# Kernel tuning notes

Hardware: AMD Instinct MI355X
Metric: run time of the kernel (lower is better)

The kernel has to match this reference:

```python
import jax, jax.numpy as jnp
import numpy as np

N_NODES = 100000
N_EDGES = 1600000
F_IN, F_HID, F_OUT = 128, 128, 16
NEG_SLOPE = 0.2


def _glorot(key, shape):
    fan = sum(shape)
    return jax.random.uniform(key, shape, jnp.float32, -1.0, 1.0) * jnp.sqrt(6.0 / fan)


def setup_inputs() -> dict:
    key = jax.random.key(0)
    ks = jax.random.split(key, 16)
    x = jax.random.normal(ks[0], (N_NODES, F_IN), jnp.float32)
    edge_index = jax.random.randint(ks[1], (2, N_EDGES), 0, N_NODES, jnp.int64)
    d1, d2, d3 = F_HID, F_HID // 2, F_OUT
    return {
        'x': x,
        'edge_index': edge_index,
        'W1': _glorot(ks[2], (F_IN, d1)), 'a_src1': _glorot(ks[3], (d1,)), 'a_dst1': _glorot(ks[4], (d1,)), 'b1': jnp.zeros((d1,), jnp.float32),
        'W2': _glorot(ks[5], (d1, d2)), 'a_src2': _glorot(ks[6], (d2,)), 'a_dst2': _glorot(ks[7], (d2,)), 'b2': jnp.zeros((d2,), jnp.float32),
        'W3': _glorot(ks[8], (d2, d3)), 'a_src3': _glorot(ks[9], (d3,)), 'a_dst3': _glorot(ks[10], (d3,)), 'b3': jnp.zeros((d3,), jnp.float32),
    }


def gat_conv(x, src, dst, W, a_s, a_d, b):
    # x: [N, Fin] -> h: [N, Fout]; src/dst: [E] (self-loops included)
    h = x @ W
    e = jax.nn.leaky_relu(h @ a_s, NEG_SLOPE * 0 + NEG_SLOPE)  # placeholder avoided below
    # attention logits per edge: leaky_relu(alpha_src[src] + alpha_dst[dst])
    al_s = h @ a_s  # [N]
    al_d = h @ a_d  # [N]
    logits = jax.nn.leaky_relu(al_s[src] + al_d[dst], NEG_SLOPE)  # [E]
    # numerically stable softmax over incoming edges of each dst node
    m = jax.ops.segment_max(logits, dst, num_segments=N_NODES)
    m = jnp.where(jnp.isfinite(m), m, 0.0)
    ex = jnp.exp(logits - m[dst])
    denom = jax.ops.segment_sum(ex, dst, num_segments=N_NODES)
    alpha = ex / denom[dst]  # self-loops guarantee denom > 0
    out = jax.ops.segment_sum(alpha[:, None] * h[src], dst, num_segments=N_NODES)
    return out + b


def reference(x, edge_index, W1, a_src1, a_dst1, b1, W2, a_src2, a_dst2, b2, W3, a_src3, a_dst3, b3):
    loops = jnp.arange(N_NODES, dtype=edge_index.dtype)
    src = jnp.concatenate([edge_index[0], loops])
    dst = jnp.concatenate([edge_index[1], loops])
    h = gat_conv(x, src, dst, W1, a_src1, a_dst1, b1)
    h = jax.nn.relu(h)  # dropout p=0.5 is identity in eval mode
    h = gat_conv(h, src, dst, W2, a_src2, a_dst2, b2)
    h = jax.nn.relu(h)
    out = gat_conv(h, src, dst, W3, a_src3, a_dst3, b3)
    return out
```

## Files before the change

### kernel.cpp

```cpp
#include <hip/hip_runtime.h>
#include <hip/hip_bf16.h>

typedef __hip_bfloat16 bf16;
typedef __attribute__((ext_vector_type(8))) __bf16 bf16x8;
typedef __attribute__((ext_vector_type(4))) float f32x4;

static constexpr int N = 100000;
static constexpr int E = 1600000;
static constexpr int ETOT = E + N;
static constexpr float SLOPE = 0.2f;

__device__ __constant__ int c_poff[12] = {0, 16384, 16512, 16640,
                                          16768, 24960, 25024, 25088,
                                          25152, 26176, 26192, 26208};
static constexpr int PTOT = 26224;
static constexpr int H_POFF[12] = {0, 16384, 16512, 16640, 16768, 24960,
                                   25024, 25088, 25152, 26176, 26192, 26208};

struct Src12 { const void* p[12]; };

__device__ __forceinline__ float bfLo(unsigned u) { return __uint_as_float(u << 16); }
__device__ __forceinline__ float bfHi(unsigned u) { return __uint_as_float(u & 0xFFFF0000u); }

__device__ __forceinline__ void fma8(const uint4 r, float e, float* acc) {
  acc[0] = fmaf(e, bfLo(r.x), acc[0]);
  acc[1] = fmaf(e, bfHi(r.x), acc[1]);
  acc[2] = fmaf(e, bfLo(r.y), acc[2]);
  acc[3] = fmaf(e, bfHi(r.y), acc[3]);
  acc[4] = fmaf(e, bfLo(r.z), acc[4]);
  acc[5] = fmaf(e, bfHi(r.z), acc[5]);
  acc[6] = fmaf(e, bfLo(r.w), acc[6]);
  acc[7] = fmaf(e, bfHi(r.w), acc[7]);
}

__device__ __forceinline__ float edge_ex(float l) {
  l = (l > 0.f) ? l : SLOPE * l;
  return __expf(l);
}

__device__ __forceinline__ void loadEdge(const int* __restrict__ ei32,
                                         const long long* __restrict__ ei64,
                                         int use64, int t, int& s, int& d) {
  if (t >= E) { s = d = t - E; return; }
  if (use64) { s = (int)ei64[t]; d = (int)ei64[E + t]; }
  else       { s = ei32[t];      d = ei32[E + t]; }
}

__device__ __forceinline__ unsigned pk2(float a, float b) {
  bf16 x = __float2bfloat16(a), y = __float2bfloat16(b);
  unsigned short ux = *(unsigned short*)&x, uy = *(unsigned short*)&y;
  return ((unsigned)uy << 16) | ux;
}

static constexpr int CHUNK = 8192;
static constexpr int NCHK  = (ETOT + CHUNK - 1) / CHUNK;
static constexpr int NB1   = (N + 511) / 512;
static constexpr int M1    = NB1 * NCHK;
static constexpr int SBLK  = (M1 + 255) / 256;

__global__ __launch_bounds__(256) void detect_kernel(
    const unsigned long long* __restrict__ ei64,
    const unsigned short* __restrict__ w1u16, int* __restrict__ flags) {
  const int t = threadIdx.x;
  __shared__ unsigned long long bl[4];
  __shared__ unsigned long long sb64;
  const int w = t >> 6;
  bool p64 = (t < 64) && (ei64[t] >= (unsigned long long)N);
  unsigned long long b64 = __ballot(p64);
  if (t == 0) sb64 = b64;
  bool pf = (((w1u16[t] >> 7) & 0xFFu) >= 126u);
  unsigned long long bf_ = __ballot(pf);
  if ((t & 63) == 0) bl[w] = bf_;
  __syncthreads();
  if (t == 0) {
    flags[0] = (sb64 == 0ull) ? 1 : 0;
    flags[1] = ((bl[0] | bl[1] | bl[2] | bl[3]) != 0ull) ? 1 : 0;
  }
}

static constexpr int PB_PAR = (PTOT + 255) / 256;
static constexpr int PB_W1  = 128 * 128 / 256;
static constexpr int PB_W2  = 128 * 64 / 256;
static constexpr int PB_W3  = 64 * 16 / 256;
static constexpr int PB_TOT = NCHK + PB_PAR + PB_W1 + PB_W2 + PB_W3;

__device__ __forceinline__ void conv_w(const void* W, int kd, int dout, int f32,
                                       bf16* __restrict__ wt, int idx) {
  int n = idx / kd, k = idx - n * kd;
  float v = f32 ? ((const float*)W)[k * dout + n]
                : __bfloat162float(((const bf16*)W)[k * dout + n]);
  wt[idx] = __float2bfloat16(v);
}

__global__ __launch_bounds__(256) void prep_kernel(
    const int* __restrict__ ei32, const long long* __restrict__ ei64,
    const int* __restrict__ flags, int* __restrict__ c1,
    Src12 s, float* __restrict__ prm,
    bf16* __restrict__ w1t, bf16* __restrict__ w2t, bf16* __restrict__ w3t) {
  const int b = blockIdx.x, tid = threadIdx.x;
  const int f64 = flags[0], f32 = flags[1];
  if (b < NCHK) {
    __shared__ int h1[NB1];
    if (tid < NB1) h1[tid] = 0;
    __syncthreads();
    const int t0 = b * CHUNK;
#pragma unroll 4
    for (int i = tid; i < CHUNK; i += 256) {
      int t = t0 + i;
      if (t < ETOT) {
        int d = (t >= E) ? (t - E) : (f64 ? (int)ei64[E + t] : ei32[E + t]);
        atomicAdd(&h1[d >> 9], 1);
      }
    }
    __syncthreads();
    if (tid < NB1) c1[tid * NCHK + b] = h1[tid];
  } else if (b < NCHK + PB_PAR) {
    int t = (b - NCHK) * 256 + tid;
    if (t < PTOT) {
      int k = 0;
#pragma unroll
      for (int i = 1; i < 12; ++i)
        if (t >= c_poff[i]) k = i;
      int j = t - c_poff[k];
      prm[t] = f32 ? ((const float*)s.p[k])[j]
                   : __bfloat162float(((const bf16*)s.p[k])[j]);
    }
  } else if (b < NCHK + PB_PAR + PB_W1) {
    conv_w(s.p[0], 128, 128, f32, w1t, (b - NCHK - PB_PAR) * 256 + tid);
  } else if (b < NCHK + PB_PAR + PB_W1 + PB_W2) {
    conv_w(s.p[4], 128, 64, f32, w2t, (b - NCHK - PB_PAR - PB_W1) * 256 + tid);
  } else {
    conv_w(s.p[8], 64, 16, f32, w3t, (b - NCHK - PB_PAR - PB_W1 - PB_W2) * 256 + tid);
  }
}

__global__ __launch_bounds__(256) void scanA_kernel(const int* __restrict__ c1,
                                                    int* __restrict__ bsum) {
  __shared__ int red[256];
  const int t = threadIdx.x;
  const int i = blockIdx.x * 256 + t;
  red[t] = (i < M1) ? c1[i] : 0;
  __syncthreads();
#pragma unroll
  for (int off = 128; off > 0; off >>= 1) {
    if (t < off) red[t] += red[t + off];
    __syncthreads();
  }
  if (t == 0) bsum[blockIdx.x] = red[0];
}

__global__ __launch_bounds__(256) void scanB_kernel(const int* __restrict__ bsum,
                                                    int* __restrict__ boff) {
  __shared__ int s[256];
  const int t = threadIdx.x;
  const int v = (t < SBLK) ? bsum[t] : 0;
  s[t] = v;
  __syncthreads();
  for (int off = 1; off < 256; off <<= 1) {
    int u = (t >= off) ? s[t - off] : 0;
    __syncthreads();
    s[t] += u;
    __syncthreads();
  }
  if (t < SBLK) boff[t] = s[t] - v;
}

__global__ __launch_bounds__(256) void scanC_kernel(const int* __restrict__ c1,
                                                    const int* __restrict__ boff,
                                                    int* __restrict__ off1) {
  __shared__ int s[256];
  const int t = threadIdx.x;
  const int i = blockIdx.x * 256 + t;
  const int v = (i < M1) ? c1[i] : 0;
  s[t] = v;
  __syncthreads();
#pragma unroll
  for (int off = 1; off < 256; off <<= 1) {
    int u = (t >= off) ? s[t - off] : 0;
    __syncthreads();
    s[t] += u;
    __syncthreads();
  }
  if (i < M1) off1[i] = boff[blockIdx.x] + s[t] - v;
}

__device__ __forceinline__ void phaseC_body(int c, const int* __restrict__ ei32,
                                            const long long* __restrict__ ei64,
                                            int f64, const int* __restrict__ off1,
                                            int2* __restrict__ tmp) {
  __shared__ int cur[NB1];
  const int tid = threadIdx.x;
  if (tid < NB1) cur[tid] = off1[tid * NCHK + c];
  __syncthreads();
  const int t0 = c * CHUNK;
#pragma unroll 4
  for (int i = tid; i < CHUNK; i += 256) {
    int t = t0 + i;
    if (t < ETOT) {
      int s, d;
      loadEdge(ei32, ei64, f64, t, s, d);
      int pos = atomicAdd(&cur[d >> 9], 1);
      tmp[pos] = make_int2(d, s);
    }
  }
}

__global__ __launch_bounds__(256) void phaseD_kernel(const int* __restrict__ off1,
                                                     const int2* __restrict__ tmp,
                                                     int* __restrict__ rowptr,
                                                     int* __restrict__ ssrt) {
  __shared__ int h2[512], e2[512], cur[512];
  __shared__ int ps[256];
  const int b = blockIdx.x, t = threadIdx.x;
  const int base = off1[b * NCHK];
  const int end = (b + 1 < NB1) ? off1[(b + 1) * NCHK] : ETOT;
  const int len = end - base;
  h2[2 * t] = 0; h2[2 * t + 1] = 0;
  __syncthreads();
  for (int i = t; i < len; i += 256)
    atomicAdd(&h2[tmp[base + i].x & 511], 1);
  __syncthreads();
  const int s1 = h2[2 * t], s2 = h2[2 * t + 1];
  ps[t] = s1 + s2;
  __syncthreads();
  for (int off = 1; off < 256; off <<= 1) {
    int u = (t >= off) ? ps[t - off] : 0;
    __syncthreads();
    ps[t] += u;
    __syncthreads();
  }
  const int ep = ps[t] - (s1 + s2);
  e2[2 * t] = ep;
  e2[2 * t + 1] = ep + s1;
  cur[2 * t] = ep;
  cur[2 * t + 1] = ep + s1;
  __syncthreads();
#pragma unroll
  for (int k = 0; k < 2; ++k) {
    int f = 2 * t + k;
    int node = (b << 9) + f;
    if (node < N) rowptr[node] = base + e2[f];
  }
  if (b == 0 && t == 0) rowptr[N] = ETOT;
  for (int i = t; i < len; i += 256) {
    int2 e = tmp[base + i];
    int pos = base + atomicAdd(&cur[e.x & 511], 1);
    ssrt[pos] = e.y;
  }
}

template <int KD, int DOUT, bool XD>
__device__ __forceinline__ void gemm_body(int bb, const void* __restrict__ inv,
                                          const int* __restrict__ flags,
                                          const unsigned short* __restrict__ wt,
                                          bf16* __restrict__ h,
                                          const float* __restrict__ a_s,
                                          const float* __restrict__ a_d,
                                          float* __restrict__ als,
                                          float* __restrict__ ald) {
  constexpr int SA = KD + 8;
  constexpr int NT = DOUT / 16;
  constexpr int KS = KD / 32;
  __shared__ unsigned short sA[64 * SA];
  __shared__ unsigned short sB[DOUT * SA];
  const int tid = threadIdx.x;
  const int m0 = bb * 64;
  for (int idx = tid; idx < DOUT * KD / 8; idx += 256) {
    int n = idx / (KD / 8), k8 = idx - n * (KD / 8);
    *(uint4*)(sB + n * SA + k8 * 8) = *(const uint4*)(wt + n * KD + k8 * 8);
  }
  const bool f32 = XD ? (flags[1] != 0) : false;
  for (int idx = tid; idx < 64 * KD / 8; idx += 256) {
    int r = idx / (KD / 8), k8 = idx - r * (KD / 8);
    int m = m0 + r;
    uint4 v = make_uint4(0, 0, 0, 0);
    if (m < N) {
      if (XD && f32) {
        const float4 v0 = *((const float4*)inv + ((size_t)m * KD + k8 * 8) / 4);
        const float4 v1 = *((const float4*)inv + ((size_t)m * KD + k8 * 8) / 4 + 1);
        v = make_uint4(pk2(v0.x, v0.y), pk2(v0.z, v0.w),
                       pk2(v1.x, v1.y), pk2(v1.z, v1.w));
      } else {
        v = *((const uint4*)inv + ((size_t)m * KD + k8 * 8) / 8);
      }
    }
    *(uint4*)(sA + r * SA + k8 * 8) = v;
  }
  __syncthreads();
  const int lane = tid & 63;
  const int wv = tid >> 6;
  const int lr = lane & 15;
  const int q = lane >> 4;
  f32x4 acc[NT];
#pragma unroll
  for (int t = 0; t < NT; ++t)
#pragma unroll
    for (int r = 0; r < 4; ++r) acc[t][r] = 0.f;
  const int arow = wv * 16 + lr;
#pragma unroll
  for (int ks = 0; ks < KS; ++ks) {
    const int k0 = ks * 32 + q * 8;
    const bf16x8 a = *(const bf16x8*)(sA + arow * SA + k0);
#pragma unroll
    for (int t = 0; t < NT; ++t) {
      const bf16x8 b = *(const bf16x8*)(sB + (t * 16 + lr) * SA + k0);
      acc[t] = __builtin_amdgcn_mfma_f32_16x16x32_bf16(a, b, acc[t], 0, 0, 0);
    }
  }
  float ps[4] = {0.f, 0.f, 0.f, 0.f}, pd[4] = {0.f, 0.f, 0.f, 0.f};
#pragma unroll
  for (int t = 0; t < NT; ++t) {
    const float av = a_s[t * 16 + lr];
    const float dv = a_d[t * 16 + lr];
#pragma unroll
    for (int r = 0; r < 4; ++r) {
      ps[r] = fmaf(acc[t][r], av, ps[r]);
      pd[r] = fmaf(acc[t][r], dv, pd[r]);
    }
  }
#pragma unroll
  for (int m = 1; m < 16; m <<= 1)
#pragma unroll
    for (int r = 0; r < 4; ++r) {
      ps[r] += __shfl_xor(ps[r], m, 64);
      pd[r] += __shfl_xor(pd[r], m, 64);
    }
  const int mb = m0 + wv * 16 + q * 4;
  if (lr == 0) {
#pragma unroll
    for (int r = 0; r < 4; ++r) {
      int m = mb + r;
      if (m < N) { als[m] = ps[r]; ald[m] = pd[r]; }
    }
  }
#pragma unroll
  for (int t = 0; t < NT; ++t)
#pragma unroll
    for (int r = 0; r < 4; ++r) {
      int m = mb + r;
      if (m < N) h[(size_t)m * DOUT + t * 16 + lr] = __float2bfloat16(acc[t][r]);
    }
}

static constexpr int GB1 = (N + 63) / 64;

__global__ __launch_bounds__(256) void gemm1_phaseC(
    const void* __restrict__ x, const int* __restrict__ flags,
    const unsigned short* __restrict__ wt, bf16* __restrict__ h,
    const float* __restrict__ a_s, const float* __restrict__ a_d,
    float* __restrict__ als, float* __restrict__ ald,
    const int* __restrict__ ei32, const long long* __restrict__ ei64,
    const int* __restrict__ off1, int2* __restrict__ tmp) {
  if (blockIdx.x < GB1) {
    gemm_body<128, 128, true>(blockIdx.x, x, flags, wt, h, a_s, a_d, als, ald);
  } else {
    int c = blockIdx.x - GB1;
    if (c < NCHK) phaseC_body(c, ei32, ei64, flags[0], off1, tmp);
  }
}

template <int KD, int DOUT>
__global__ __launch_bounds__(256, 8) void agg_gemm(
    const int* __restrict__ rowptr, const int* __restrict__ ssrt,
    const float* __restrict__ als_in, const float* __restrict__ ald_in,
    const unsigned short* __restrict__ hb, const float* __restrict__ bias_in,
    const unsigned short* __restrict__ wt, bf16* __restrict__ hout,
    const float* __restrict__ a_s, const float* __restrict__ a_d,
    float* __restrict__ als_out, float* __restrict__ ald_out) {
  constexpr int SA = KD + 8;
  constexpr int NT = DOUT / 16;
  constexpr int KS = KD / 32;
  constexpr int TPN = KD / 8;
  constexpr int NPB = 256 / TPN;
  constexpr int NBAT = 64 / NPB;
  __shared__ unsigned short sA[64 * SA];
  const int tid = threadIdx.x;
  const int m0 = blockIdx.x * 64;
  const int sub = tid % TPN;
  const int rb = tid / TPN;
  const int col0 = sub * 8;
#pragma unroll
  for (int bat = 0; bat < NBAT; ++bat) {
    const int r = bat * NPB + rb;
    const int d = m0 + r;
    uint4 w = make_uint4(0, 0, 0, 0);
    if (d < N) {
      const int p0 = rowptr[d], p1 = rowptr[d + 1];
      const float ad = ald_in[d];
      float acc[8];
#pragma unroll
      for (int c = 0; c < 8; ++c) acc[c] = 0.f;
      float sum = 0.f;
      int p = p0;
      for (; p + 4 <= p1; p += 4) {
        const int s0 = ssrt[p + 0];
        const int s1 = ssrt[p + 1];
        const int s2 = ssrt[p + 2];
        const int s3 = ssrt[p + 3];
        const uint4 r0 = *reinterpret_cast<const uint4*>(hb + (size_t)s0 * KD + col0);
        const uint4 r1 = *reinterpret_cast<const uint4*>(hb + (size_t)s1 * KD + col0);
        const uint4 r2 = *reinterpret_cast<const uint4*>(hb + (size_t)s2 * KD + col0);
        const uint4 r3 = *reinterpret_cast<const uint4*>(hb + (size_t)s3 * KD + col0);
        const float x0 = edge_ex(als_in[s0] + ad);
        const float x1 = edge_ex(als_in[s1] + ad);
        const float x2 = edge_ex(als_in[s2] + ad);
        const float x3 = edge_ex(als_in[s3] + ad);
        sum += (x0 + x1) + (x2 + x3);
        fma8(r0, x0, acc);
        fma8(r1, x1, acc);
        fma8(r2, x2, acc);
        fma8(r3, x3, acc);
      }
      for (; p < p1; ++p) {
        const int s = ssrt[p];
        const uint4 rr = *reinterpret_cast<const uint4*>(hb + (size_t)s * KD + col0);
        const float x = edge_ex(als_in[s] + ad);
        sum += x;
        fma8(rr, x, acc);
      }
      const float inv = 1.f / sum;
      float v[8];
#pragma unroll
      for (int c = 0; c < 8; ++c) {
        float t = acc[c] * inv + bias_in[col0 + c];
        v[c] = (t > 0.f) ? t : 0.f;
      }
      w = make_uint4(pk2(v[0], v[1]), pk2(v[2], v[3]),
                     pk2(v[4], v[5]), pk2(v[6], v[7]));
    }
    *(uint4*)(sA + r * SA + col0) = w;
  }
  __syncthreads();
  const int lane = tid & 63;
  const int wv = tid >> 6;
  const int lr = lane & 15;
  const int q = lane >> 4;
  f32x4 acc[NT];
#pragma unroll
  for (int t = 0; t < NT; ++t)
#pragma unroll
    for (int r = 0; r < 4; ++r) acc[t][r] = 0.f;
  const int arow = wv * 16 + lr;
#pragma unroll
  for (int ks = 0; ks < KS; ++ks) {
    const int k0 = ks * 32 + q * 8;
    const bf16x8 a = *(const bf16x8*)(sA + arow * SA + k0);
#pragma unroll
    for (int t = 0; t < NT; ++t) {
      const bf16x8 b = *(const bf16x8*)(wt + (t * 16 + lr) * KD + k0);
      acc[t] = __builtin_amdgcn_mfma_f32_16x16x32_bf16(a, b, acc[t], 0, 0, 0);
    }
  }
  float ps[4] = {0.f, 0.f, 0.f, 0.f}, pd[4] = {0.f, 0.f, 0.f, 0.f};
#pragma unroll
  for (int t = 0; t < NT; ++t) {
    const float av = a_s[t * 16 + lr];
    const float dv = a_d[t * 16 + lr];
#pragma unroll
    for (int r = 0; r < 4; ++r) {
      ps[r] = fmaf(acc[t][r], av, ps[r]);
      pd[r] = fmaf(acc[t][r], dv, pd[r]);
    }
  }
#pragma unroll
  for (int m = 1; m < 16; m <<= 1)
#pragma unroll
    for (int r = 0; r < 4; ++r) {
      ps[r] += __shfl_xor(ps[r], m, 64);
      pd[r] += __shfl_xor(pd[r], m, 64);
    }
  const int mb = m0 + wv * 16 + q * 4;
  if (lr == 0) {
#pragma unroll
    for (int r = 0; r < 4; ++r) {
      int m = mb + r;
      if (m < N) { als_out[m] = ps[r]; ald_out[m] = pd[r]; }
    }
  }
#pragma unroll
  for (int t = 0; t < NT; ++t)
#pragma unroll
    for (int r = 0; r < 4; ++r) {
      int m = mb + r;
      if (m < N) hout[(size_t)m * DOUT + t * 16 + lr] = __float2bfloat16(acc[t][r]);
    }
}

template <int DOUT, bool RELU, bool FINAL>
__global__ __launch_bounds__(256) void aggregate_csr(const int* __restrict__ rowptr,
                                                     const int* __restrict__ ssrt,
                                                     const float* __restrict__ als,
                                                     const float* __restrict__ ald,
                                                     const unsigned short* __restrict__ hb,
                                                     const float* __restrict__ bias,
                                                     bf16* __restrict__ outb,
                                                     void* __restrict__ outv,
                                                     const int* __restrict__ flags) {
  constexpr int TPN = DOUT / 8;
  constexpr int NPB = 256 / TPN;
  const int sub = threadIdx.x % TPN;
  const int d = blockIdx.x * NPB + threadIdx.x / TPN;
  if (d >= N) return;
  const int p0 = rowptr[d], p1 = rowptr[d + 1];
  const float ad = ald[d];
  const int col0 = sub * 8;
  float acc[8];
#pragma unroll
  for (int c = 0; c < 8; ++c) acc[c] = 0.f;
  float sum = 0.f;
  int p = p0;
  for (; p + 4 <= p1; p += 4) {
    const int s0 = ssrt[p + 0];
    const int s1 = ssrt[p + 1];
    const int s2 = ssrt[p + 2];
    const int s3 = ssrt[p + 3];
    const uint4 r0 = *reinterpret_cast<const uint4*>(hb + (size_t)s0 * DOUT + col0);
    const uint4 r1 = *reinterpret_cast<const uint4*>(hb + (size_t)s1 * DOUT + col0);
    const uint4 r2 = *reinterpret_cast<const uint4*>(hb + (size_t)s2 * DOUT + col0);
    const uint4 r3 = *reinterpret_cast<const uint4*>(hb + (size_t)s3 * DOUT + col0);
    const float x0 = edge_ex(als[s0] + ad);
    const float x1 = edge_ex(als[s1] + ad);
    const float x2 = edge_ex(als[s2] + ad);
    const float x3 = edge_ex(als[s3] + ad);
    sum += (x0 + x1) + (x2 + x3);
    fma8(r0, x0, acc);
    fma8(r1, x1, acc);
    fma8(r2, x2, acc);
    fma8(r3, x3, acc);
  }
  for (; p < p1; ++p) {
    const int s = ssrt[p];
    const uint4 r = *reinterpret_cast<const uint4*>(hb + (size_t)s * DOUT + col0);
    const float x = edge_ex(als[s] + ad);
    sum += x;
    fma8(r, x, acc);
  }
  const float inv = 1.f / sum;
  if (FINAL) {
    const bool f32o = flags[1] != 0;
#pragma unroll
    for (int c = 0; c < 8; ++c) {
      float v = acc[c] * inv + bias[col0 + c];
      if (f32o) ((float*)outv)[(size_t)d * DOUT + col0 + c] = v;
      else      ((bf16*)outv)[(size_t)d * DOUT + col0 + c] = __float2bfloat16(v);
    }
  } else {
#pragma unroll
    for (int c = 0; c < 8; ++c) {
      float v = acc[c] * inv + bias[col0 + c];
      if (RELU) v = (v > 0.f) ? v : 0.f;
      outb[(size_t)d * DOUT + col0 + c] = __float2bfloat16(v);
    }
  }
}

static inline size_t rup(size_t v) { return (v + 255) & ~(size_t)255; }

extern "C" void kernel_launch(void* const* d_in, const int* in_sizes, int n_in,
                              void* d_out, int out_size, void* d_ws, size_t ws_size,
                              hipStream_t stream) {
  const int* ei32 = (const int*)d_in[1];
  const long long* ei64 = (const long long*)d_in[1];

  char* p = (char*)d_ws;
  int*   flags  = (int*)p;   p += 256;
  float* prm    = (float*)p; p += rup((size_t)PTOT * 4);
  bf16*  w1t    = (bf16*)p;  p += rup((size_t)128 * 128 * 2);
  bf16*  w2t    = (bf16*)p;  p += rup((size_t)128 * 64 * 2);
  bf16*  w3t    = (bf16*)p;  p += rup((size_t)64 * 16 * 2);
  float* als1   = (float*)p; p += rup((size_t)N * 4);
  float* ald1   = (float*)p; p += rup((size_t)N * 4);
  float* als2   = (float*)p; p += rup((size_t)N * 4);
  float* ald2   = (float*)p; p += rup((size_t)N * 4);
  int*   rowptr = (int*)p;   p += rup((size_t)(N + 1) * 4);
  int*   c1     = (int*)p;   p += rup((size_t)M1 * 4);
  int*   off1   = (int*)p;   p += rup((size_t)M1 * 4);
  int*   bsum   = (int*)p;   p += rup((size_t)SBLK * 4);
  int*   boff   = (int*)p;   p += rup((size_t)SBLK * 4);
  int2*  tmp    = (int2*)p;  p += rup((size_t)ETOT * 8);
  int*   ssrt   = (int*)p;   p += rup((size_t)ETOT * 4);
  bf16*  h1     = (bf16*)p;  p += rup((size_t)N * 128 * 2);
  bf16*  h2     = (bf16*)p;  p += rup((size_t)N * 64 * 2);
  bf16*  h3     = (bf16*)p;

  Src12 s;
  for (int i = 0; i < 12; ++i) s.p[i] = d_in[2 + i];

  detect_kernel<<<1, 256, 0, stream>>>(
      (const unsigned long long*)d_in[1], (const unsigned short*)d_in[2], flags);
  prep_kernel<<<PB_TOT, 256, 0, stream>>>(ei32, ei64, flags, c1, s, prm, w1t, w2t, w3t);
  scanA_kernel<<<SBLK, 256, 0, stream>>>(c1, bsum);
  scanB_kernel<<<1, 256, 0, stream>>>(bsum, boff);
  scanC_kernel<<<SBLK, 256, 0, stream>>>(c1, boff, off1);

  const float *as1 = prm + H_POFF[1], *ad1 = prm + H_POFF[2], *b1 = prm + H_POFF[3];
  const float *as2 = prm + H_POFF[5], *ad2 = prm + H_POFF[6], *b2 = prm + H_POFF[7];
  const float *as3 = prm + H_POFF[9], *ad3 = prm + H_POFF[10], *b3 = prm + H_POFF[11];

  gemm1_phaseC<<<GB1 + NCHK, 256, 0, stream>>>(
      d_in[0], flags, (const unsigned short*)w1t, h1, as1, ad1, als1, ald1,
      ei32, ei64, off1, tmp);
  phaseD_kernel<<<NB1, 256, 0, stream>>>(off1, tmp, rowptr, ssrt);
  agg_gemm<128, 64><<<GB1, 256, 0, stream>>>(
      rowptr, ssrt, als1, ald1, (const unsigned short*)h1, b1,
      (const unsigned short*)w2t, h2, as2, ad2, als2, ald2);
  agg_gemm<64, 16><<<GB1, 256, 0, stream>>>(
      rowptr, ssrt, als2, ald2, (const unsigned short*)h2, b2,
      (const unsigned short*)w3t, h3, as3, ad3, als1, ald1);
  aggregate_csr<16, false, true><<<(N + 127) / 128, 256, 0, stream>>>(
      rowptr, ssrt, als1, ald1, (const unsigned short*)h3, b3, nullptr, d_out, flags);
}
```

Before: 324.4 us.

## Dynamic row scheduling and deeper edge unroll in agg_gemm; narrower final aggregate

In agg_gemm, the fixed per-thread-group row batches are replaced with a shared-memory atomic counter, so each group of TPN lanes claims the next destination row dynamically. This balances the uneven in-degrees within a block. The edge loop gains an 8-way unrolled path that issues more independent gathers before consuming them, and the launch-bounds occupancy hint drops from 8 to 6 to allow more registers. The final 16-wide aggregation now uses 4 columns per thread with uint2 loads and twice as many blocks, which increases parallelism per node at the cost of more redundant index and logit loads.

```diff
diff --git a/kernel.cpp b/kernel.cpp
--- a/kernel.cpp
+++ b/kernel.cpp
@@ -31,6 +31,13 @@
   acc[5] = fmaf(e, bfHi(r.z), acc[5]);
   acc[6] = fmaf(e, bfLo(r.w), acc[6]);
   acc[7] = fmaf(e, bfHi(r.w), acc[7]);
+}
+
+__device__ __forceinline__ void fma4(const uint2 r, float e, float* acc) {
+  acc[0] = fmaf(e, bfLo(r.x), acc[0]);
+  acc[1] = fmaf(e, bfHi(r.x), acc[1]);
+  acc[2] = fmaf(e, bfLo(r.y), acc[2]);
+  acc[3] = fmaf(e, bfHi(r.y), acc[3]);
 }
 
 __device__ __forceinline__ float edge_ex(float l) {
@@ -360,7 +367,7 @@
 }
 
 template <int KD, int DOUT>
-__global__ __launch_bounds__(256, 8) void agg_gemm(
+__global__ __launch_bounds__(256, 6) void agg_gemm(
     const int* __restrict__ rowptr, const int* __restrict__ ssrt,
     const float* __restrict__ als_in, const float* __restrict__ ald_in,
     const unsigned short* __restrict__ hb, const float* __restrict__ bias_in,
@@ -371,17 +378,20 @@
   constexpr int NT = DOUT / 16;
   constexpr int KS = KD / 32;
   constexpr int TPN = KD / 8;
-  constexpr int NPB = 256 / TPN;
-  constexpr int NBAT = 64 / NPB;
   __shared__ unsigned short sA[64 * SA];
+  __shared__ int sCur;
   const int tid = threadIdx.x;
   const int m0 = blockIdx.x * 64;
+  if (tid == 0) sCur = 0;
+  __syncthreads();
   const int sub = tid % TPN;
-  const int rb = tid / TPN;
   const int col0 = sub * 8;
-#pragma unroll
-  for (int bat = 0; bat < NBAT; ++bat) {
-    const int r = bat * NPB + rb;
+  const int ldr = (tid & 63) & ~(TPN - 1);
+  for (;;) {
+    int rv = 0;
+    if (sub == 0) rv = atomicAdd(&sCur, 1);
+    const int r = __shfl(rv, ldr, 64);
+    if (r >= 64) break;
     const int d = m0 + r;
     uint4 w = make_uint4(0, 0, 0, 0);
     if (d < N) {
@@ -392,6 +402,18 @@
       for (int c = 0; c < 8; ++c) acc[c] = 0.f;
       float sum = 0.f;
       int p = p0;
+      for (; p + 8 <= p1; p += 8) {
+        int sv[8]; uint4 rr[8]; float xv[8];
+#pragma unroll
+        for (int u = 0; u < 8; ++u) sv[u] = ssrt[p + u];
+#pragma unroll
+        for (int u = 0; u < 8; ++u)
+          rr[u] = *reinterpret_cast<const uint4*>(hb + (size_t)sv[u] * KD + col0);
+#pragma unroll
+        for (int u = 0; u < 8; ++u) xv[u] = edge_ex(als_in[sv[u]] + ad);
+#pragma unroll
+        for (int u = 0; u < 8; ++u) { sum += xv[u]; fma8(rr[u], xv[u], acc); }
+      }
       for (; p + 4 <= p1; p += 4) {
         const int s0 = ssrt[p + 0];
         const int s1 = ssrt[p + 1];
@@ -496,17 +518,18 @@
                                                      bf16* __restrict__ outb,
                                                      void* __restrict__ outv,
                                                      const int* __restrict__ flags) {
-  constexpr int TPN = DOUT / 8;
+  constexpr int V = (DOUT >= 64) ? 8 : 4;
+  constexpr int TPN = DOUT / V;
   constexpr int NPB = 256 / TPN;
   const int sub = threadIdx.x % TPN;
   const int d = blockIdx.x * NPB + threadIdx.x / TPN;
   if (d >= N) return;
   const int p0 = rowptr[d], p1 = rowptr[d + 1];
   const float ad = ald[d];
-  const int col0 = sub * 8;
-  float acc[8];
-#pragma unroll
-  for (int c = 0; c < 8; ++c) acc[c] = 0.f;
+  const int col0 = sub * V;
+  float acc[V];
+#pragma unroll
+  for (int c = 0; c < V; ++c) acc[c] = 0.f;
   float sum = 0.f;
   int p = p0;
   for (; p + 4 <= p1; p += 4) {
@@ -514,39 +537,55 @@
     const int s1 = ssrt[p + 1];
     const int s2 = ssrt[p + 2];
     const int s3 = ssrt[p + 3];
-    const uint4 r0 = *reinterpret_cast<const uint4*>(hb + (size_t)s0 * DOUT + col0);
-    const uint4 r1 = *reinterpret_cast<const uint4*>(hb + (size_t)s1 * DOUT + col0);
-    const uint4 r2 = *reinterpret_cast<const uint4*>(hb + (size_t)s2 * DOUT + col0);
-    const uint4 r3 = *reinterpret_cast<const uint4*>(hb + (size_t)s3 * DOUT + col0);
     const float x0 = edge_ex(als[s0] + ad);
     const float x1 = edge_ex(als[s1] + ad);
     const float x2 = edge_ex(als[s2] + ad);
     const float x3 = edge_ex(als[s3] + ad);
     sum += (x0 + x1) + (x2 + x3);
-    fma8(r0, x0, acc);
-    fma8(r1, x1, acc);
-    fma8(r2, x2, acc);
-    fma8(r3, x3, acc);
+    if constexpr (V == 8) {
+      const uint4 r0 = *reinterpret_cast<const uint4*>(hb + (size_t)s0 * DOUT + col0);
+      const uint4 r1 = *reinterpret_cast<const uint4*>(hb + (size_t)s1 * DOUT + col0);
+      const uint4 r2 = *reinterpret_cast<const uint4*>(hb + (size_t)s2 * DOUT + col0);
+      const uint4 r3 = *reinterpret_cast<const uint4*>(hb + (size_t)s3 * DOUT + col0);
+      fma8(r0, x0, acc);
+      fma8(r1, x1, acc);
+      fma8(r2, x2, acc);
+      fma8(r3, x3, acc);
+    } else {
+      const uint2 r0 = *reinterpret_cast<const uint2*>(hb + (size_t)s0 * DOUT + col0);
+      const uint2 r1 = *reinterpret_cast<const uint2*>(hb + (size_t)s1 * DOUT + col0);
+      const uint2 r2 = *reinterpret_cast<const uint2*>(hb + (size_t)s2 * DOUT + col0);
+      const uint2 r3 = *reinterpret_cast<const uint2*>(hb + (size_t)s3 * DOUT + col0);
+      fma4(r0, x0, acc);
+      fma4(r1, x1, acc);
+      fma4(r2, x2, acc);
+      fma4(r3, x3, acc);
+    }
   }
   for (; p < p1; ++p) {
     const int s = ssrt[p];
-    const uint4 r = *reinterpret_cast<const uint4*>(hb + (size_t)s * DOUT + col0);
     const float x = edge_ex(als[s] + ad);
     sum += x;
-    fma8(r, x, acc);
+    if constexpr (V == 8) {
+      const uint4 r = *reinterpret_cast<const uint4*>(hb + (size_t)s * DOUT + col0);
+      fma8(r, x, acc);
+    } else {
+      const uint2 r = *reinterpret_cast<const uint2*>(hb + (size_t)s * DOUT + col0);
+      fma4(r, x, acc);
+    }
   }
   const float inv = 1.f / sum;
   if (FINAL) {
     const bool f32o = flags[1] != 0;
 #pragma unroll
-    for (int c = 0; c < 8; ++c) {
+    for (int c = 0; c < V; ++c) {
       float v = acc[c] * inv + bias[col0 + c];
       if (f32o) ((float*)outv)[(size_t)d * DOUT + col0 + c] = v;
       else      ((bf16*)outv)[(size_t)d * DOUT + col0 + c] = __float2bfloat16(v);
     }
   } else {
 #pragma unroll
-    for (int c = 0; c < 8; ++c) {
+    for (int c = 0; c < V; ++c) {
       float v = acc[c] * inv + bias[col0 + c];
       if (RELU) v = (v > 0.f) ? v : 0.f;
       outb[(size_t)d * DOUT + col0 + c] = __float2bfloat16(v);
@@ -607,6 +646,6 @@
   agg_gemm<64, 16><<<GB1, 256, 0, stream>>>(
       rowptr, ssrt, als2, ald2, (const unsigned short*)h2, b2,
       (const unsigned short*)w3t, h3, as3, ad3, als1, ald1);
-  aggregate_csr<16, false, true><<<(N + 127) / 128, 256, 0, stream>>>(
+  aggregate_csr<16, false, true><<<(N + 63) / 64, 256, 0, stream>>>(
       rowptr, ssrt, als1, ald1, (const unsigned short*)h3, b3, nullptr, d_out, flags);
 }
```

Result: slower. 404.8 us (+24.8%).
